# Performance work log

Measured on AMD Instinct MI355X. Metric: run time of the kernel, lower is better.

## Reference

```python
import jax, jax.numpy as jnp
import numpy as np

B, N, F, H = 2, 256, 64, 4
HID = 64            # hidden_features
C = H * HID         # n_coefficients = 256
KF = 50             # kernel_features (rbf count)
CUTOFF_UPPER = 5.0  # ExpNormalSmearing default (lower = 0)
ALPHA = 5.0 / CUTOFF_UPPER


def _dense(key, din, dout):
    scale = 1.0 / np.sqrt(din)
    return jax.random.uniform(key, (din, dout), minval=-scale, maxval=scale).astype(jnp.float32)


def setup_inputs() -> dict:
    key = jax.random.key(0)
    ks = jax.random.split(key, 16)
    start = float(np.exp(-CUTOFF_UPPER))
    means = jnp.asarray(np.linspace(start, 1.0, KF), jnp.float32)
    betas = jnp.full((KF,), (2.0 / KF * (1.0 - start)) ** -2, dtype=jnp.float32)
    d_edge_in = 2 * F              # h_cat_ht width
    d_cat = 2 * F + KF + 1         # concat([h0, rbf*h, dist])
    return dict(
        h=jax.random.normal(ks[0], (B, N, F), jnp.float32),
        x=jax.random.normal(ks[1], (B, N, 3), jnp.float32),
        v=jax.random.normal(ks[2], (B, N, 3), jnp.float32) * 0.1,
        W_in=_dense(ks[3], d_edge_in, KF), b_in=jnp.zeros((KF,), jnp.float32),
        rbf_means=means, rbf_betas=betas,
        W_o1=_dense(ks[4], d_cat, HID), b_o1=jnp.zeros((HID,), jnp.float32),
        W_o2=_dense(ks[5], HID, HID), b_o2=jnp.zeros((HID,), jnp.float32),
        W_sem=_dense(ks[6], HID, H), b_sem=jnp.zeros((H,), jnp.float32),
        W_xmix=_dense(ks[7], C, C),
        W_p1=_dense(ks[8], C, HID), b_p1=jnp.zeros((HID,), jnp.float32),
        W_p2=_dense(ks[9], HID, HID), b_p2=jnp.zeros((HID,), jnp.float32),
        W_n1=_dense(ks[10], F + C + HID, HID), b_n1=jnp.zeros((HID,), jnp.float32),
        W_n2=_dense(ks[11], HID, F), b_n2=jnp.zeros((F,), jnp.float32),
        W_v1=_dense(ks[12], F, HID), b_v1=jnp.zeros((HID,), jnp.float32),
        W_v2=_dense(ks[13], HID, 1),
        W_vmix=_dense(ks[14], C, 1),
    )


def reference(h, x, v, W_in, b_in, rbf_means, rbf_betas, W_o1, b_o1, W_o2, b_o2,
              W_sem, b_sem, W_xmix, W_p1, b_p1, W_p2, b_p2,
              W_n1, b_n1, W_n2, b_n2, W_v1, b_v1, W_v2, W_vmix):
    silu = jax.nn.silu
    n = h.shape[-2]
    # all-pairs displacements: entry [i, j] = x_j - x_i  (get_x_minus_xt)
    x_minus_xt = x[..., None, :, :] - x[..., :, None, :]                       # [B,N,N,3]
    d = jnp.sqrt(jax.nn.relu((x_minus_xt ** 2).sum(-1, keepdims=True)) + 1e-5)  # [B,N,N,1]
    # h_cat_ht: concat([h_j, h_i]) per pair (get_h_cat_ht)
    h_j = jnp.broadcast_to(h[..., None, :, :], h.shape[:-2] + (n, n, h.shape[-1]))
    h_i = jnp.broadcast_to(h[..., :, None, :], h.shape[:-2] + (n, n, h.shape[-1]))
    h_cat = jnp.concatenate([h_j, h_i], -1)                                     # [B,N,N,2F]
    # --- edge model: ContinuousFilterConvolutionWithConcatenation ---
    h1 = h_cat @ W_in + b_in                                                    # [B,N,N,KF]
    cut = 0.5 * (jnp.cos(d * jnp.pi / CUTOFF_UPPER) + 1.0) * (d < CUTOFF_UPPER)
    rbf = cut * jnp.exp(-rbf_betas * (jnp.exp(-ALPHA * d) - rbf_means) ** 2)    # [B,N,N,KF]
    h_e_mtx = silu(jnp.concatenate([h_cat, rbf * h1, d], -1) @ W_o1 + b_o1) @ W_o2 + b_o2  # [B,N,N,HID]
    # --- semantic attention (cutoff=None => euclidean factor is 1.0) ---
    att = jax.nn.celu(h_e_mtx @ W_sem + b_sem, alpha=2.0)                       # [B,N,N,H]
    att = att - 1e5 * jnp.eye(n, dtype=att.dtype)[..., None]                    # mask self-pairs
    att = jax.nn.softmax(att, axis=-2)
    combined = att / att.sum(-2, keepdims=True)                                 # combined_attention
    # per-head weighted edge features, flattened (feature-major, head-minor)
    h_e_att = (h_e_mtx[..., :, None] * combined[..., None, :]).reshape(h_e_mtx.shape[:-1] + (C,))  # [B,N,N,C]
    # --- spatial attention ---
    coeff = jnp.tanh(h_e_att @ W_xmix)                                          # x_mixing, [B,N,N,C]
    x_hat = x_minus_xt / (d + 1e-5)                                             # [B,N,N,3]
    # combinations[b,i,j,c,:] = x_hat[b,i,j,:] * coeff[b,i,j,c]; mean over j, fused:
    comb_sum = jnp.einsum('bijc,bijd->bicd', coeff, x_hat) / n                  # [B,N,C,3]
    comb_norm = (comb_sum ** 2).sum(-1)                                         # [B,N,C]
    h_comb = silu(silu(comb_norm @ W_p1 + b_p1) @ W_p2 + b_p2)                  # post_norm_mlp
    # --- aggregate + node model (residual) ---
    h_e = h_e_att.sum(-2)                                                       # [B,N,C]
    h_new = h + silu(silu(jnp.concatenate([h, h_e, h_comb], -1) @ W_n1 + b_n1) @ W_n2 + b_n2)
    # --- velocity / coordinate update (v_mixing then mean over j, fused via comb_sum) ---
    delta_v = jnp.einsum('bicd,c->bid', comb_sum, W_vmix[:, 0])                 # [B,N,3]
    v_scale = 2.0 * jax.nn.sigmoid(silu(h_new @ W_v1 + b_v1) @ W_v2)            # velocity_mlp + double_sigmoid
    v_new = delta_v + v_scale * v
    x_new = x + v_new
    return (h_new, x_new, v_new)
```

## Files before the change

### kernel.cpp

```cpp
#include <hip/hip_runtime.h>
#include <hip/hip_bf16.h>

typedef __hip_bfloat16 bf16;
typedef __attribute__((ext_vector_type(8))) short bf16x8;
typedef __attribute__((ext_vector_type(4))) short s16x4;
typedef __attribute__((ext_vector_type(4))) float f32x4;

#define NNODE 512

__device__ __forceinline__ float b2f(bf16 v){ return __bfloat162float(v); }
__device__ __forceinline__ float siluf(float x){ return x / (1.f + __expf(-x)); }
__device__ __forceinline__ float tanhfast(float x){ return 1.f - 2.f/(__expf(2.f*x)+1.f); }
__device__ __forceinline__ float celu2(float x){ return x > 0.f ? x : 2.f*(__expf(0.5f*x)-1.f); }
__device__ __forceinline__ float bs2f(short v){ union{unsigned int i; float f;} t; t.i = ((unsigned int)(unsigned short)v) << 16; return t.f; }
__device__ __forceinline__ short f2bs(float x){ union{ bf16 b; short s; } u; u.b = __float2bfloat16(x); return u.s; }
__device__ __forceinline__ float lo16f(unsigned int u){ union{unsigned int i; float f;} t; t.i = u<<16; return t.f; }
__device__ __forceinline__ float hi16f(unsigned int u){ union{unsigned int i; float f;} t; t.i = u & 0xffff0000u; return t.f; }

template<typename T> __device__ __forceinline__ float ldv(const void* p, int i);
template<> __device__ __forceinline__ float ldv<float>(const void* p, int i){ return ((const float*)p)[i]; }
template<> __device__ __forceinline__ float ldv<bf16 >(const void* p, int i){ return b2f(((const bf16*)p)[i]); }

template<typename T> __device__ __forceinline__ void stv(void* p, int i, float v);
template<> __device__ __forceinline__ void stv<float>(void* p, int i, float v){ ((float*)p)[i] = v; }
template<> __device__ __forceinline__ void stv<bf16 >(void* p, int i, float v){ ((bf16*)p)[i] = __float2bfloat16(v); }

template<typename T> __device__ __forceinline__ short ldbs(const void* p, int i);
template<> __device__ __forceinline__ short ldbs<bf16 >(const void* p, int i){ union{ bf16 b; short s; } u; u.b = ((const bf16*)p)[i]; return u.s; }
template<> __device__ __forceinline__ short ldbs<float>(const void* p, int i){ return f2bs(((const float*)p)[i]); }

struct Args {
    const void *h,*x,*v,*Win,*bin,*means,*betas,*Wo1,*bo1,*Wo2,*bo2,*Wsem,*bsem,*Wx,
               *Wp1,*bp1,*Wp2,*bp2,*Wn1,*bn1,*Wn2,*bn2,*Wv1,*bv1,*Wv2,*Wvm;
};

__device__ __forceinline__ bool detect_f32(const void* means){
    float v = b2f(((const bf16*)means)[0]);
    return (fabsf(v) > 1.0f || v != v);
}

template<typename T>
__device__ __forceinline__ void nodepre_body(const Args& A, short* __restrict__ U1,
                                             float* __restrict__ Aj, short* __restrict__ WxT,
                                             float* sh, float (*p1)[64], float (*p2)[64])
{
    int bn = blockIdx.x, tid = threadIdx.x;
    int t = tid & 63, ks = tid >> 6;
    if (tid < 64) sh[tid] = ldv<T>(A.h, bn*64 + tid);
    __syncthreads();
    float a1 = 0.f;
    #pragma unroll
    for (int q = 0; q < 16; ++q){
        int f = ks*16 + q;
        a1 += sh[f] * ldv<T>(A.Wo1, f*64 + t);
    }
    p1[ks][t] = a1;
    if (t < 50){
        float a2 = 0.f;
        #pragma unroll
        for (int q = 0; q < 16; ++q){
            int f = ks*16 + q;
            a2 += sh[f] * ldv<T>(A.Win, f*50 + t);
        }
        p2[ks][t] = a2;
    }
    if (tid < 128){
        int oo = bn*128 + tid;
        int hh = oo >> 14, rem = oo & 16383, n = rem >> 6, f = oo & 63;
        WxT[oo] = ldbs<T>(A.Wx, (4*f + hh)*256 + n);
    }
    __syncthreads();
    if (tid < 64){
        U1[bn*64 + tid] = f2bs(p1[0][tid] + p1[1][tid] + p1[2][tid] + p1[3][tid]);
        float av = (tid < 50) ? (p2[0][tid] + p2[1][tid] + p2[2][tid] + p2[3][tid]) : 0.f;
        Aj[bn*64 + tid] = av;
    }
}

__global__ void __launch_bounds__(256) k_nodepre(Args A, short* __restrict__ U1,
                                                 float* __restrict__ Aj, short* __restrict__ WxT)
{
    __shared__ float sh[64];
    __shared__ float p1[4][64];
    __shared__ float p2[4][64];
    if (detect_f32(A.means)) nodepre_body<float>(A, U1, Aj, WxT, sh, p1, p2);
    else                     nodepre_body<bf16 >(A, U1, Aj, WxT, sh, p1, p2);
}

struct SmemPost {
    __align__(16) float att[256][4];
    float part[4][256];
    float red[768];
    float cn[256];
    float he[256];
    float fa[64];
    float fb[64];
    float mpart[8][64];
    float tmp[8][4];
};
struct Smem {
    __align__(16) bf16  e[256][72];
    __align__(16) float x4[256][4];
    float hi[64];
    float ub[64];
    float wl[64];
    __align__(16) float kc[64][4];
    short wsem[256];
    __align__(16) short wo1t[64*72];
    __align__(16) short wo2t[64*72];
    union {
        SmemPost post;
        __align__(16) short mid[8][16][72];
    } u;
};

template<typename T>
__device__ __forceinline__ void sake_body(const Args& A,
        const short* __restrict__ U1w, const float* __restrict__ Ajw,
        const short* __restrict__ wxt, void* __restrict__ out, Smem& S)
{
    int bi = blockIdx.x;
    int b = bi >> 8, i = bi & 255;
    int tid = threadIdx.x, w = tid >> 6, lane = tid & 63;
    int lane15 = lane & 15, quad = lane >> 4;

    if (tid < 64)  S.hi[tid]   = ldv<T>(A.h, bi*64 + tid);
    if (tid < 256) S.wsem[tid] = ldbs<T>(A.Wsem, tid);
    if (tid < 64){
        bool kv = tid < 50;
        S.kc[tid][0] = kv ? ldv<T>(A.means, tid) : 0.f;
        S.kc[tid][1] = kv ? ldv<T>(A.betas, tid) : 0.f;
        S.kc[tid][2] = kv ? ldv<T>(A.bin,   tid) : 0.f;
        S.kc[tid][3] = 0.f;
    }
    #pragma unroll
    for (int q = 0; q < 8; ++q){
        int idx = q*512 + tid;
        int n = idx >> 6, k = idx & 63;
        S.wo2t[n*72 + k] = ldbs<T>(A.Wo2, k*64 + n);
        S.wo1t[n*72 + k] = (k < 50) ? ldbs<T>(A.Wo1, (128+k)*64 + n) : (short)0;
    }
    float xi0 = ldv<T>(A.x, bi*3+0), xi1 = ldv<T>(A.x, bi*3+1), xi2 = ldv<T>(A.x, bi*3+2);
    if (tid < 256){
        int j = tid;
        float dx = ldv<T>(A.x,(b*256+j)*3+0) - xi0;
        float dy = ldv<T>(A.x,(b*256+j)*3+1) - xi1;
        float dz = ldv<T>(A.x,(b*256+j)*3+2) - xi2;
        float dd = sqrtf(dx*dx + dy*dy + dz*dz + 1e-5f);
        float inv = 1.f/(dd + 1e-5f);
        S.x4[j][0] = dx*inv; S.x4[j][1] = dy*inv; S.x4[j][2] = dz*inv; S.x4[j][3] = dd;
    }
    __syncthreads();

    if (w == 0){
        float u2v = 0.f;
        for (int f = 0; f < 64; ++f) u2v += S.hi[f] * ldv<T>(A.Wo1, (64+f)*64 + lane);
        S.ub[lane] = u2v + ldv<T>(A.bo1, lane);
        S.wl[lane] = ldv<T>(A.Wo1, 178*64 + lane);
    } else if (w == 1 && lane < 50){
        float av = 0.f;
        for (int f = 0; f < 64; ++f) av += S.hi[f] * ldv<T>(A.Win, (64+f)*50 + lane);
        S.kc[lane][3] = av;
    }
    __syncthreads();

    float ubr[16], wlr[16], bo2r[16];
    #pragma unroll
    for (int nf = 0; nf < 4; ++nf){
        #pragma unroll
        for (int r = 0; r < 4; ++r){
            int m = nf*16 + quad*4 + r;
            ubr[nf*4+r]  = S.ub[m];
            wlr[nf*4+r]  = S.wl[m];
            bo2r[nf*4+r] = ldv<T>(A.bo2, m);
        }
    }

    for (int pass = 0; pass < 2; ++pass){
        int j = pass*128 + w*16 + lane15;
        float dd  = S.x4[j][3];
        float cut = (dd < 5.f) ? 0.5f*(__cosf(dd*0.6283185307f) + 1.f) : 0.f;
        float ed  = __expf(-dd);
        const float* ajp = Ajw + (b*256 + j)*64;
        bf16x8 Brb[2];
        #pragma unroll
        for (int s = 0; s < 2; ++s){
            int kb = s*32 + quad*8;
            f32x4 a0 = *(const f32x4*)(ajp + kb);
            f32x4 a1 = *(const f32x4*)(ajp + kb + 4);
            bf16x8 bv;
            #pragma unroll
            for (int i2 = 0; i2 < 8; ++i2){
                int k = kb + i2;
                f32x4 kcv = *(const f32x4*)&S.kc[k][0];
                float aj = (i2 < 4) ? a0[i2] : a1[i2-4];
                float h1 = aj + kcv[3] + kcv[2];
                float ex = ed - kcv[0];
                float val = cut * __expf(-kcv[1]*ex*ex) * h1;
                bv[i2] = (k < 50) ? f2bs(val) : (short)0;
            }
            Brb[s] = bv;
        }
        const short* u1p = U1w + (b*256 + j)*64;
        #pragma unroll
        for (int nf = 0; nf < 4; ++nf){
            const short* wp = S.wo1t + (nf*16 + lane15)*72;
            bf16x8 A0 = *(const bf16x8*)(wp + quad*8);
            bf16x8 A1 = *(const bf16x8*)(wp + 32 + quad*8);
            s16x4 u4 = *(const s16x4*)(u1p + nf*16 + quad*4);
            f32x4 C;
            #pragma unroll
            for (int r = 0; r < 4; ++r)
                C[r] = bs2f(u4[r]) + ubr[nf*4+r] + dd*wlr[nf*4+r];
            C = __builtin_amdgcn_mfma_f32_16x16x32_bf16(A0, Brb[0], C, 0, 0, 0);
            C = __builtin_amdgcn_mfma_f32_16x16x32_bf16(A1, Brb[1], C, 0, 0, 0);
            s16x4 m4;
            #pragma unroll
            for (int r = 0; r < 4; ++r) m4[r] = f2bs(siluf(C[r]));
            *(s16x4*)&S.u.mid[w][lane15][nf*16 + quad*4] = m4;
        }
        bf16x8 Bm0 = *(const bf16x8*)&S.u.mid[w][lane15][quad*8];
        bf16x8 Bm1 = *(const bf16x8*)&S.u.mid[w][lane15][32 + quad*8];
        #pragma unroll
        for (int nf = 0; nf < 4; ++nf){
            const short* wp = S.wo2t + (nf*16 + lane15)*72;
            bf16x8 A0 = *(const bf16x8*)(wp + quad*8);
            bf16x8 A1 = *(const bf16x8*)(wp + 32 + quad*8);
            f32x4 C = (f32x4){bo2r[nf*4+0], bo2r[nf*4+1], bo2r[nf*4+2], bo2r[nf*4+3]};
            C = __builtin_amdgcn_mfma_f32_16x16x32_bf16(A0, Bm0, C, 0, 0, 0);
            C = __builtin_amdgcn_mfma_f32_16x16x32_bf16(A1, Bm1, C, 0, 0, 0);
            s16x4 e4;
            #pragma unroll
            for (int r = 0; r < 4; ++r) e4[r] = f2bs(C[r]);
            *(s16x4*)&((short*)S.e)[j*72 + nf*16 + quad*4] = e4;
        }
    }
    __syncthreads();

    {
        bf16x8 Bs[2];
        #pragma unroll
        for (int ks = 0; ks < 2; ++ks){
            bf16x8 bv = (bf16x8){0,0,0,0,0,0,0,0};
            if (lane15 < 4){
                #pragma unroll
                for (int i2 = 0; i2 < 8; ++i2)
                    bv[i2] = S.wsem[(ks*32 + quad*8 + i2)*4 + lane15];
            }
            Bs[ks] = bv;
        }
        float bsv = (lane15 < 4) ? ldv<T>(A.bsem, lane15) : 0.f;
        #pragma unroll
        for (int t2 = 0; t2 < 2; ++t2){
            int jt = w*2 + t2;
            const short* ep = (const short*)S.e + (jt*16 + lane15)*72;
            bf16x8 A0 = *(const bf16x8*)(ep + quad*8);
            bf16x8 A1 = *(const bf16x8*)(ep + 32 + quad*8);
            f32x4 C = (f32x4){bsv, bsv, bsv, bsv};
            C = __builtin_amdgcn_mfma_f32_16x16x32_bf16(A0, Bs[0], C, 0, 0, 0);
            C = __builtin_amdgcn_mfma_f32_16x16x32_bf16(A1, Bs[1], C, 0, 0, 0);
            if (lane15 < 4){
                #pragma unroll
                for (int r = 0; r < 4; ++r){
                    int jr = jt*16 + quad*4 + r;
                    float lv = celu2(C[r]);
                    if (jr == i) lv -= 1e5f;
                    S.u.post.att[jr][lane15] = lv;
                }
            }
        }
    }
    __syncthreads();

    float ex0 = 0.f, ex1 = 0.f, ex2 = 0.f, ex3 = 0.f;
    if (tid < 256){
        float l0 = S.u.post.att[tid][0], l1 = S.u.post.att[tid][1];
        float l2 = S.u.post.att[tid][2], l3 = S.u.post.att[tid][3];
        float m0 = l0, m1 = l1, m2 = l2, m3 = l3;
        #pragma unroll
        for (int off = 1; off < 64; off <<= 1){
            m0 = fmaxf(m0, __shfl_xor(m0, off)); m1 = fmaxf(m1, __shfl_xor(m1, off));
            m2 = fmaxf(m2, __shfl_xor(m2, off)); m3 = fmaxf(m3, __shfl_xor(m3, off));
        }
        if (lane == 0){
            S.u.post.tmp[w][0] = m0; S.u.post.tmp[w][1] = m1;
            S.u.post.tmp[w][2] = m2; S.u.post.tmp[w][3] = m3;
        }
        ex0 = l0; ex1 = l1; ex2 = l2; ex3 = l3;
    }
    __syncthreads();
    if (tid < 256){
        float m0 = fmaxf(fmaxf(S.u.post.tmp[0][0], S.u.post.tmp[1][0]), fmaxf(S.u.post.tmp[2][0], S.u.post.tmp[3][0]));
        float m1 = fmaxf(fmaxf(S.u.post.tmp[0][1], S.u.post.tmp[1][1]), fmaxf(S.u.post.tmp[2][1], S.u.post.tmp[3][1]));
        float m2 = fmaxf(fmaxf(S.u.post.tmp[0][2], S.u.post.tmp[1][2]), fmaxf(S.u.post.tmp[2][2], S.u.post.tmp[3][2]));
        float m3 = fmaxf(fmaxf(S.u.post.tmp[0][3], S.u.post.tmp[1][3]), fmaxf(S.u.post.tmp[2][3], S.u.post.tmp[3][3]));
        ex0 = __expf(ex0-m0); ex1 = __expf(ex1-m1); ex2 = __expf(ex2-m2); ex3 = __expf(ex3-m3);
        float s0 = ex0, s1 = ex1, s2 = ex2, s3 = ex3;
        #pragma unroll
        for (int off = 1; off < 64; off <<= 1){
            s0 += __shfl_xor(s0, off); s1 += __shfl_xor(s1, off);
            s2 += __shfl_xor(s2, off); s3 += __shfl_xor(s3, off);
        }
        if (lane == 0){
            S.u.post.tmp[4+w][0] = s0; S.u.post.tmp[4+w][1] = s1;
            S.u.post.tmp[4+w][2] = s2; S.u.post.tmp[4+w][3] = s3;
        }
    }
    __syncthreads();
    if (tid < 256){
        float s0 = S.u.post.tmp[4][0]+S.u.post.tmp[5][0]+S.u.post.tmp[6][0]+S.u.post.tmp[7][0];
        float s1 = S.u.post.tmp[4][1]+S.u.post.tmp[5][1]+S.u.post.tmp[6][1]+S.u.post.tmp[7][1];
        float s2 = S.u.post.tmp[4][2]+S.u.post.tmp[5][2]+S.u.post.tmp[6][2]+S.u.post.tmp[7][2];
        float s3 = S.u.post.tmp[4][3]+S.u.post.tmp[5][3]+S.u.post.tmp[6][3]+S.u.post.tmp[7][3];
        S.u.post.att[tid][0] = ex0/s0; S.u.post.att[tid][1] = ex1/s1;
        S.u.post.att[tid][2] = ex2/s2; S.u.post.att[tid][3] = ex3/s3;
    }
    __syncthreads();

    {
        int cg = tid & 127, js = tid >> 7;
        int fp = cg >> 2, hh = cg & 3;
        float acc0 = 0.f, acc1 = 0.f;
        const unsigned int* ep = (const unsigned int*)S.e;
        for (int jj = 0; jj < 64; ++jj){
            int j = js*64 + jj;
            unsigned int u = ep[j*36 + fp];
            float a = S.u.post.att[j][hh];
            acc0 += lo16f(u)*a; acc1 += hi16f(u)*a;
        }
        S.u.post.part[js][8*fp + hh]     = acc0;
        S.u.post.part[js][8*fp + 4 + hh] = acc1;
    }
    __syncthreads();
    if (tid < 256)
        S.u.post.he[tid] = S.u.post.part[0][tid] + S.u.post.part[1][tid]
                         + S.u.post.part[2][tid] + S.u.post.part[3][tid];

    {
        const short* se_s = (const short*)S.e;
        bf16x8 Bh[2][4][2];
        #pragma unroll
        for (int nf2 = 0; nf2 < 2; ++nf2){
            int n = w*32 + nf2*16 + lane15;
            #pragma unroll
            for (int hh = 0; hh < 4; ++hh){
                const short* bp = wxt + (hh*256 + n)*64 + quad*8;
                Bh[nf2][hh][0] = *(const bf16x8*)(bp);
                Bh[nf2][hh][1] = *(const bf16x8*)(bp + 32);
            }
        }
        float ca[2][3];
        #pragma unroll
        for (int nf2 = 0; nf2 < 2; ++nf2){ ca[nf2][0]=0.f; ca[nf2][1]=0.f; ca[nf2][2]=0.f; }

        for (int mt = 0; mt < 16; ++mt){
            int jq = mt*16 + quad*4;
            f32x4 att4[4];
            #pragma unroll
            for (int r = 0; r < 4; ++r) att4[r] = *(const f32x4*)&S.u.post.att[jq + r][0];
            bf16x8 Af[2];
            #pragma unroll
            for (int ks = 0; ks < 2; ++ks)
                Af[ks] = *(const bf16x8*)(se_s + (mt*16 + lane15)*72 + ks*32 + quad*8);
            #pragma unroll
            for (int nf2 = 0; nf2 < 2; ++nf2){
                float Pt[4] = {0.f, 0.f, 0.f, 0.f};
                #pragma unroll
                for (int hh = 0; hh < 4; ++hh){
                    f32x4 Cc = (f32x4){0.f,0.f,0.f,0.f};
                    Cc = __builtin_amdgcn_mfma_f32_16x16x32_bf16(Af[0], Bh[nf2][hh][0], Cc, 0, 0, 0);
                    Cc = __builtin_amdgcn_mfma_f32_16x16x32_bf16(Af[1], Bh[nf2][hh][1], Cc, 0, 0, 0);
                    #pragma unroll
                    for (int r = 0; r < 4; ++r) Pt[r] += att4[r][hh] * Cc[r];
                }
                #pragma unroll
                for (int r = 0; r < 4; ++r){
                    int j = jq + r;
                    float cf = tanhfast(Pt[r]);
                    f32x4 xh = *(const f32x4*)&S.x4[j][0];
                    ca[nf2][0] += cf*xh[0]; ca[nf2][1] += cf*xh[1]; ca[nf2][2] += cf*xh[2];
                }
            }
        }
        #pragma unroll
        for (int nf2 = 0; nf2 < 2; ++nf2){
            #pragma unroll
            for (int d = 0; d < 3; ++d){
                float vs = ca[nf2][d];
                vs += __shfl_xor(vs, 16);
                vs += __shfl_xor(vs, 32);
                if (quad == 0) S.u.post.red[(w*32 + nf2*16 + lane15)*3 + d] = vs;
            }
        }
    }
    __syncthreads();

    const float sc = 1.f/256.f;
    if (tid < 256){
        float c0 = S.u.post.red[tid*3+0]*sc, c1 = S.u.post.red[tid*3+1]*sc, c2 = S.u.post.red[tid*3+2]*sc;
        S.u.post.cn[tid] = c0*c0 + c1*c1 + c2*c2;
    }
    __syncthreads();

    {
        float acc = 0.f;
        int c0 = w*32;
        for (int c = c0; c < c0+32; ++c) acc += S.u.post.cn[c] * ldv<T>(A.Wp1, c*64 + lane);
        S.u.post.mpart[w][lane] = acc;
    }
    __syncthreads();
    if (tid < 64){
        float acc = ldv<T>(A.bp1, tid);
        #pragma unroll
        for (int q = 0; q < 8; ++q) acc += S.u.post.mpart[q][tid];
        S.u.post.fa[tid] = siluf(acc);
    }
    __syncthreads();
    {
        float acc = 0.f;
        int k0 = w*8;
        #pragma unroll
        for (int k = 0; k < 8; ++k) acc += S.u.post.fa[k0+k] * ldv<T>(A.Wp2, (k0+k)*64 + lane);
        S.u.post.mpart[w][lane] = acc;
    }
    __syncthreads();
    if (tid < 64){
        float acc = ldv<T>(A.bp2, tid);
        #pragma unroll
        for (int q = 0; q < 8; ++q) acc += S.u.post.mpart[q][tid];
        S.u.post.fb[tid] = siluf(acc);
    }
    __syncthreads();
    {
        float acc = 0.f;
        int r0 = w*48;
        for (int r = r0; r < r0+48; ++r){
            float xv = (r < 64) ? S.hi[r] : (r < 320) ? S.u.post.he[r-64] : S.u.post.fb[r-320];
            acc += xv * ldv<T>(A.Wn1, r*64 + lane);
        }
        S.u.post.mpart[w][lane] = acc;
    }
    __syncthreads();
    if (tid < 64){
        float acc = ldv<T>(A.bn1, tid);
        #pragma unroll
        for (int q = 0; q < 8; ++q) acc += S.u.post.mpart[q][tid];
        S.u.post.fa[tid] = siluf(acc);
    }
    __syncthreads();
    {
        float acc = 0.f;
        int k0 = w*8;
        #pragma unroll
        for (int k = 0; k < 8; ++k) acc += S.u.post.fa[k0+k] * ldv<T>(A.Wn2, (k0+k)*64 + lane);
        S.u.post.mpart[w][lane] = acc;
    }
    __syncthreads();
    if (tid < 64){
        float acc = ldv<T>(A.bn2, tid);
        #pragma unroll
        for (int q = 0; q < 8; ++q) acc += S.u.post.mpart[q][tid];
        float hn = S.hi[tid] + siluf(acc);
        stv<T>(out, bi*64 + tid, hn);
        S.u.post.fb[tid] = hn;
    }
    __syncthreads();
    {
        float acc = 0.f;
        int k0 = w*8;
        #pragma unroll
        for (int k = 0; k < 8; ++k) acc += S.u.post.fb[k0+k] * ldv<T>(A.Wv1, (k0+k)*64 + lane);
        S.u.post.mpart[w][lane] = acc;
    }
    __syncthreads();
    float vscale = 0.f;
    if (tid < 64){
        float acc = ldv<T>(A.bv1, tid);
        #pragma unroll
        for (int q = 0; q < 8; ++q) acc += S.u.post.mpart[q][tid];
        float term = siluf(acc) * ldv<T>(A.Wv2, tid);
        #pragma unroll
        for (int off = 1; off < 64; off <<= 1) term += __shfl_xor(term, off);
        vscale = 2.f / (1.f + __expf(-term));
    }
    if (w < 4){
        int c = w*64 + lane;
        float wv = ldv<T>(A.Wvm, c);
        float d0 = S.u.post.red[c*3+0]*sc*wv;
        float d1 = S.u.post.red[c*3+1]*sc*wv;
        float d2 = S.u.post.red[c*3+2]*sc*wv;
        #pragma unroll
        for (int off = 1; off < 64; off <<= 1){
            d0 += __shfl_xor(d0, off); d1 += __shfl_xor(d1, off); d2 += __shfl_xor(d2, off);
        }
        if (lane == 0){ S.u.post.tmp[w][0] = d0; S.u.post.tmp[w][1] = d1; S.u.post.tmp[w][2] = d2; }
    }
    __syncthreads();
    if (tid < 3){
        float dv = S.u.post.tmp[0][tid] + S.u.post.tmp[1][tid] + S.u.post.tmp[2][tid] + S.u.post.tmp[3][tid];
        float vn = dv + vscale * ldv<T>(A.v, bi*3 + tid);
        float xn = ldv<T>(A.x, bi*3 + tid) + vn;
        stv<T>(out, 32768 + bi*3 + tid, xn);
        stv<T>(out, 34304 + bi*3 + tid, vn);
    }
}

__global__ void __launch_bounds__(512, 4) k_sake(Args A,
                                                 const short* __restrict__ U1w,
                                                 const float* __restrict__ Ajw,
                                                 const short* __restrict__ wxt,
                                                 void* __restrict__ out)
{
    __shared__ Smem S;
    if (detect_f32(A.means)) sake_body<float>(A, U1w, Ajw, wxt, out, S);
    else                     sake_body<bf16 >(A, U1w, Ajw, wxt, out, S);
}

extern "C" void kernel_launch(void* const* d_in, const int* in_sizes, int n_in,
                              void* d_out, int out_size, void* d_ws, size_t ws_size,
                              hipStream_t stream)
{
    Args A;
    A.h     = d_in[0];  A.x     = d_in[1];  A.v     = d_in[2];
    A.Win   = d_in[3];  A.bin   = d_in[4];  A.means = d_in[5];  A.betas = d_in[6];
    A.Wo1   = d_in[7];  A.bo1   = d_in[8];  A.Wo2   = d_in[9];  A.bo2   = d_in[10];
    A.Wsem  = d_in[11]; A.bsem  = d_in[12]; A.Wx    = d_in[13];
    A.Wp1   = d_in[14]; A.bp1   = d_in[15]; A.Wp2   = d_in[16]; A.bp2   = d_in[17];
    A.Wn1   = d_in[18]; A.bn1   = d_in[19]; A.Wn2   = d_in[20]; A.bn2   = d_in[21];
    A.Wv1   = d_in[22]; A.bv1   = d_in[23]; A.Wv2   = d_in[24]; A.Wvm   = d_in[25];

    short* U1b  = (short*)d_ws;
    float* Aj   = (float*)((char*)d_ws + 65536);
    short* WxT  = (short*)((char*)d_ws + 65536 + 131072);

    k_nodepre<<<NNODE, 256, 0, stream>>>(A, U1b, Aj, WxT);
    k_sake<<<NNODE, 512, 0, stream>>>(A, U1b, Aj, WxT, d_out);
}
```

Measured before the change: 180.1 us.

## Fold h_e aggregation into Wn1 via MFMA and slim post-MLP barriers

Precomputes transposed Wn1 slices (hi/lo bf16 split) alongside WxT so the attention-weighted h_e sum is folded directly into the Wn1 product using MFMA, removing the scalar 256-wide h_e reduction and part buffers. Stores attention weights in padding columns of the edge tile to shrink shared memory, unions edge weights with post buffers, and removes two barriers. Post-MLPs are restructured to use shuffle reductions across 8 output features per wave instead of cross-wave smem partials. Risks precision changes from hi/lo split and possible race from removed barriers.

```diff
diff --git a/kernel.cpp b/kernel.cpp
--- a/kernel.cpp
+++ b/kernel.cpp
@@ -64,10 +64,21 @@
         }
         p2[ks][t] = a2;
     }
-    if (tid < 128){
-        int oo = bn*128 + tid;
-        int hh = oo >> 14, rem = oo & 16383, n = rem >> 6, f = oo & 63;
-        WxT[oo] = ldbs<T>(A.Wx, (4*f + hh)*256 + n);
+    if (tid < 192){
+        int oo = bn*192 + tid;
+        int hh = oo / 24576;
+        int rem = oo - hh*24576;
+        int n = rem >> 6, k = rem & 63;
+        short v;
+        if (n < 256){
+            v = ldbs<T>(A.Wx, (4*k + hh)*256 + n);
+        } else if (n < 320){
+            v = ldbs<T>(A.Wn1, (64 + 4*k + hh)*64 + (n - 256));
+        } else {
+            float wv = ldv<T>(A.Wn1, (64 + 4*k + hh)*64 + (n - 320));
+            v = f2bs(wv - bs2f(f2bs(wv)));
+        }
+        WxT[oo] = v;
     }
     __syncthreads();
     if (tid < 64){
@@ -88,15 +99,18 @@
 }
 
 struct SmemPost {
-    __align__(16) float att[256][4];
-    float part[4][256];
     float red[768];
     float cn[256];
-    float he[256];
     float fa[64];
     float fb[64];
-    float mpart[8][64];
+    float hep[8][16];
     float tmp[8][4];
+    float tmp2[8];
+};
+struct SmemEdge {
+    __align__(16) short wo1t[64*72];
+    __align__(16) short wo2t[64*72];
+    __align__(16) short mid[8][16][72];
 };
 struct Smem {
     __align__(16) bf16  e[256][72];
@@ -105,14 +119,13 @@
     float ub[64];
     float wl[64];
     __align__(16) float kc[64][4];
-    short wsem[256];
-    __align__(16) short wo1t[64*72];
-    __align__(16) short wo2t[64*72];
-    union {
-        SmemPost post;
-        __align__(16) short mid[8][16][72];
-    } u;
+    __align__(16) short wsem[256];
+    union { SmemEdge edge; SmemPost post; } u;
 };
+
+__device__ __forceinline__ float* attp(Smem& S, int j){
+    return (float*)((short*)S.e + j*72 + 64);
+}
 
 template<typename T>
 __device__ __forceinline__ void sake_body(const Args& A,
@@ -131,14 +144,14 @@
         S.kc[tid][0] = kv ? ldv<T>(A.means, tid) : 0.f;
         S.kc[tid][1] = kv ? ldv<T>(A.betas, tid) : 0.f;
         S.kc[tid][2] = kv ? ldv<T>(A.bin,   tid) : 0.f;
-        S.kc[tid][3] = 0.f;
+        if (!kv) S.kc[tid][3] = 0.f;
     }
     #pragma unroll
     for (int q = 0; q < 8; ++q){
         int idx = q*512 + tid;
         int n = idx >> 6, k = idx & 63;
-        S.wo2t[n*72 + k] = ldbs<T>(A.Wo2, k*64 + n);
-        S.wo1t[n*72 + k] = (k < 50) ? ldbs<T>(A.Wo1, (128+k)*64 + n) : (short)0;
+        S.u.edge.wo2t[n*72 + k] = ldbs<T>(A.Wo2, k*64 + n);
+        S.u.edge.wo1t[n*72 + k] = (k < 50) ? ldbs<T>(A.Wo1, (128+k)*64 + n) : (short)0;
     }
     float xi0 = ldv<T>(A.x, bi*3+0), xi1 = ldv<T>(A.x, bi*3+1), xi2 = ldv<T>(A.x, bi*3+2);
     if (tid < 256){
@@ -150,16 +163,14 @@
         float inv = 1.f/(dd + 1e-5f);
         S.x4[j][0] = dx*inv; S.x4[j][1] = dy*inv; S.x4[j][2] = dz*inv; S.x4[j][3] = dd;
     }
-    __syncthreads();
-
     if (w == 0){
         float u2v = 0.f;
-        for (int f = 0; f < 64; ++f) u2v += S.hi[f] * ldv<T>(A.Wo1, (64+f)*64 + lane);
+        for (int f = 0; f < 64; ++f) u2v += ldv<T>(A.h, bi*64 + f) * ldv<T>(A.Wo1, (64+f)*64 + lane);
         S.ub[lane] = u2v + ldv<T>(A.bo1, lane);
         S.wl[lane] = ldv<T>(A.Wo1, 178*64 + lane);
     } else if (w == 1 && lane < 50){
         float av = 0.f;
-        for (int f = 0; f < 64; ++f) av += S.hi[f] * ldv<T>(A.Win, (64+f)*50 + lane);
+        for (int f = 0; f < 64; ++f) av += ldv<T>(A.h, bi*64 + f) * ldv<T>(A.Win, (64+f)*50 + lane);
         S.kc[lane][3] = av;
     }
     __syncthreads();
@@ -176,6 +187,7 @@
         }
     }
 
+    #pragma unroll
     for (int pass = 0; pass < 2; ++pass){
         int j = pass*128 + w*16 + lane15;
         float dd  = S.x4[j][3];
@@ -204,7 +216,7 @@
         const short* u1p = U1w + (b*256 + j)*64;
         #pragma unroll
         for (int nf = 0; nf < 4; ++nf){
-            const short* wp = S.wo1t + (nf*16 + lane15)*72;
+            const short* wp = S.u.edge.wo1t + (nf*16 + lane15)*72;
             bf16x8 A0 = *(const bf16x8*)(wp + quad*8);
             bf16x8 A1 = *(const bf16x8*)(wp + 32 + quad*8);
             s16x4 u4 = *(const s16x4*)(u1p + nf*16 + quad*4);
@@ -217,13 +229,13 @@
             s16x4 m4;
             #pragma unroll
             for (int r = 0; r < 4; ++r) m4[r] = f2bs(siluf(C[r]));
-            *(s16x4*)&S.u.mid[w][lane15][nf*16 + quad*4] = m4;
-        }
-        bf16x8 Bm0 = *(const bf16x8*)&S.u.mid[w][lane15][quad*8];
-        bf16x8 Bm1 = *(const bf16x8*)&S.u.mid[w][lane15][32 + quad*8];
+            *(s16x4*)&S.u.edge.mid[w][lane15][nf*16 + quad*4] = m4;
+        }
+        bf16x8 Bm0 = *(const bf16x8*)&S.u.edge.mid[w][lane15][quad*8];
+        bf16x8 Bm1 = *(const bf16x8*)&S.u.edge.mid[w][lane15][32 + quad*8];
         #pragma unroll
         for (int nf = 0; nf < 4; ++nf){
-            const short* wp = S.wo2t + (nf*16 + lane15)*72;
+            const short* wp = S.u.edge.wo2t + (nf*16 + lane15)*72;
             bf16x8 A0 = *(const bf16x8*)(wp + quad*8);
             bf16x8 A1 = *(const bf16x8*)(wp + 32 + quad*8);
             f32x4 C = (f32x4){bo2r[nf*4+0], bo2r[nf*4+1], bo2r[nf*4+2], bo2r[nf*4+3]};
@@ -235,7 +247,6 @@
             *(s16x4*)&((short*)S.e)[j*72 + nf*16 + quad*4] = e4;
         }
     }
-    __syncthreads();
 
     {
         bf16x8 Bs[2];
@@ -252,7 +263,7 @@
         float bsv = (lane15 < 4) ? ldv<T>(A.bsem, lane15) : 0.f;
         #pragma unroll
         for (int t2 = 0; t2 < 2; ++t2){
-            int jt = w*2 + t2;
+            int jt = t2 ? (8 + w) : w;
             const short* ep = (const short*)S.e + (jt*16 + lane15)*72;
             bf16x8 A0 = *(const bf16x8*)(ep + quad*8);
             bf16x8 A1 = *(const bf16x8*)(ep + 32 + quad*8);
@@ -265,7 +276,7 @@
                     int jr = jt*16 + quad*4 + r;
                     float lv = celu2(C[r]);
                     if (jr == i) lv -= 1e5f;
-                    S.u.post.att[jr][lane15] = lv;
+                    attp(S, jr)[lane15] = lv;
                 }
             }
         }
@@ -274,9 +285,8 @@
 
     float ex0 = 0.f, ex1 = 0.f, ex2 = 0.f, ex3 = 0.f;
     if (tid < 256){
-        float l0 = S.u.post.att[tid][0], l1 = S.u.post.att[tid][1];
-        float l2 = S.u.post.att[tid][2], l3 = S.u.post.att[tid][3];
-        float m0 = l0, m1 = l1, m2 = l2, m3 = l3;
+        f32x4 l = *(const f32x4*)attp(S, tid);
+        float m0 = l[0], m1 = l[1], m2 = l[2], m3 = l[3];
         #pragma unroll
         for (int off = 1; off < 64; off <<= 1){
             m0 = fmaxf(m0, __shfl_xor(m0, off)); m1 = fmaxf(m1, __shfl_xor(m1, off));
@@ -286,7 +296,7 @@
             S.u.post.tmp[w][0] = m0; S.u.post.tmp[w][1] = m1;
             S.u.post.tmp[w][2] = m2; S.u.post.tmp[w][3] = m3;
         }
-        ex0 = l0; ex1 = l1; ex2 = l2; ex3 = l3;
+        ex0 = l[0]; ex1 = l[1]; ex2 = l[2]; ex3 = l[3];
     }
     __syncthreads();
     if (tid < 256){
@@ -312,86 +322,87 @@
         float s1 = S.u.post.tmp[4][1]+S.u.post.tmp[5][1]+S.u.post.tmp[6][1]+S.u.post.tmp[7][1];
         float s2 = S.u.post.tmp[4][2]+S.u.post.tmp[5][2]+S.u.post.tmp[6][2]+S.u.post.tmp[7][2];
         float s3 = S.u.post.tmp[4][3]+S.u.post.tmp[5][3]+S.u.post.tmp[6][3]+S.u.post.tmp[7][3];
-        S.u.post.att[tid][0] = ex0/s0; S.u.post.att[tid][1] = ex1/s1;
-        S.u.post.att[tid][2] = ex2/s2; S.u.post.att[tid][3] = ex3/s3;
-    }
-    __syncthreads();
-
-    {
-        int cg = tid & 127, js = tid >> 7;
-        int fp = cg >> 2, hh = cg & 3;
-        float acc0 = 0.f, acc1 = 0.f;
-        const unsigned int* ep = (const unsigned int*)S.e;
-        for (int jj = 0; jj < 64; ++jj){
-            int j = js*64 + jj;
-            unsigned int u = ep[j*36 + fp];
-            float a = S.u.post.att[j][hh];
-            acc0 += lo16f(u)*a; acc1 += hi16f(u)*a;
-        }
-        S.u.post.part[js][8*fp + hh]     = acc0;
-        S.u.post.part[js][8*fp + 4 + hh] = acc1;
-    }
-    __syncthreads();
-    if (tid < 256)
-        S.u.post.he[tid] = S.u.post.part[0][tid] + S.u.post.part[1][tid]
-                         + S.u.post.part[2][tid] + S.u.post.part[3][tid];
+        *(f32x4*)attp(S, tid) = (f32x4){ex0/s0, ex1/s1, ex2/s2, ex3/s3};
+    }
+    __syncthreads();
 
     {
         const short* se_s = (const short*)S.e;
-        bf16x8 Bh[2][4][2];
         #pragma unroll
         for (int nf2 = 0; nf2 < 2; ++nf2){
             int n = w*32 + nf2*16 + lane15;
+            bf16x8 Bh[4][2];
             #pragma unroll
             for (int hh = 0; hh < 4; ++hh){
-                const short* bp = wxt + (hh*256 + n)*64 + quad*8;
-                Bh[nf2][hh][0] = *(const bf16x8*)(bp);
-                Bh[nf2][hh][1] = *(const bf16x8*)(bp + 32);
-            }
-        }
-        float ca[2][3];
-        #pragma unroll
-        for (int nf2 = 0; nf2 < 2; ++nf2){ ca[nf2][0]=0.f; ca[nf2][1]=0.f; ca[nf2][2]=0.f; }
-
-        for (int mt = 0; mt < 16; ++mt){
-            int jq = mt*16 + quad*4;
-            f32x4 att4[4];
-            #pragma unroll
-            for (int r = 0; r < 4; ++r) att4[r] = *(const f32x4*)&S.u.post.att[jq + r][0];
-            bf16x8 Af[2];
-            #pragma unroll
-            for (int ks = 0; ks < 2; ++ks)
-                Af[ks] = *(const bf16x8*)(se_s + (mt*16 + lane15)*72 + ks*32 + quad*8);
-            #pragma unroll
-            for (int nf2 = 0; nf2 < 2; ++nf2){
+                const short* bp = wxt + (hh*384 + n)*64 + quad*8;
+                Bh[hh][0] = *(const bf16x8*)(bp);
+                Bh[hh][1] = *(const bf16x8*)(bp + 32);
+            }
+            float c0 = 0.f, c1 = 0.f, c2 = 0.f;
+            for (int mt = 0; mt < 16; ++mt){
+                int jq = mt*16 + quad*4;
+                f32x4 att4[4];
+                #pragma unroll
+                for (int r = 0; r < 4; ++r) att4[r] = *(const f32x4*)attp(S, jq + r);
+                bf16x8 Af[2];
+                #pragma unroll
+                for (int ks = 0; ks < 2; ++ks)
+                    Af[ks] = *(const bf16x8*)(se_s + (mt*16 + lane15)*72 + ks*32 + quad*8);
                 float Pt[4] = {0.f, 0.f, 0.f, 0.f};
                 #pragma unroll
                 for (int hh = 0; hh < 4; ++hh){
                     f32x4 Cc = (f32x4){0.f,0.f,0.f,0.f};
-                    Cc = __builtin_amdgcn_mfma_f32_16x16x32_bf16(Af[0], Bh[nf2][hh][0], Cc, 0, 0, 0);
-                    Cc = __builtin_amdgcn_mfma_f32_16x16x32_bf16(Af[1], Bh[nf2][hh][1], Cc, 0, 0, 0);
+                    Cc = __builtin_amdgcn_mfma_f32_16x16x32_bf16(Af[0], Bh[hh][0], Cc, 0, 0, 0);
+                    Cc = __builtin_amdgcn_mfma_f32_16x16x32_bf16(Af[1], Bh[hh][1], Cc, 0, 0, 0);
                     #pragma unroll
                     for (int r = 0; r < 4; ++r) Pt[r] += att4[r][hh] * Cc[r];
                 }
                 #pragma unroll
                 for (int r = 0; r < 4; ++r){
-                    int j = jq + r;
                     float cf = tanhfast(Pt[r]);
-                    f32x4 xh = *(const f32x4*)&S.x4[j][0];
-                    ca[nf2][0] += cf*xh[0]; ca[nf2][1] += cf*xh[1]; ca[nf2][2] += cf*xh[2];
+                    f32x4 xh = *(const f32x4*)&S.x4[jq + r][0];
+                    c0 += cf*xh[0]; c1 += cf*xh[1]; c2 += cf*xh[2];
                 }
             }
-        }
-        #pragma unroll
-        for (int nf2 = 0; nf2 < 2; ++nf2){
-            #pragma unroll
-            for (int d = 0; d < 3; ++d){
-                float vs = ca[nf2][d];
-                vs += __shfl_xor(vs, 16);
-                vs += __shfl_xor(vs, 32);
-                if (quad == 0) S.u.post.red[(w*32 + nf2*16 + lane15)*3 + d] = vs;
-            }
-        }
+            c0 += __shfl_xor(c0, 16); c0 += __shfl_xor(c0, 32);
+            c1 += __shfl_xor(c1, 16); c1 += __shfl_xor(c1, 32);
+            c2 += __shfl_xor(c2, 16); c2 += __shfl_xor(c2, 32);
+            if (quad == 0){
+                S.u.post.red[n*3 + 0] = c0;
+                S.u.post.red[n*3 + 1] = c1;
+                S.u.post.red[n*3 + 2] = c2;
+            }
+        }
+    }
+
+    {
+        const short* se_s = (const short*)S.e;
+        int t16 = (w >> 1) * 16;
+        int mt0 = (w & 1) * 8;
+        float heacc = 0.f;
+        #pragma unroll
+        for (int hh = 0; hh < 4; ++hh){
+            const short* bhp = wxt + (hh*384 + 256 + t16 + lane15)*64 + quad*8;
+            bf16x8 Bhi0 = *(const bf16x8*)(bhp);
+            bf16x8 Bhi1 = *(const bf16x8*)(bhp + 32);
+            bf16x8 Blo0 = *(const bf16x8*)(bhp + 4096);
+            bf16x8 Blo1 = *(const bf16x8*)(bhp + 4096 + 32);
+            for (int mt = mt0; mt < mt0 + 8; ++mt){
+                bf16x8 Af0 = *(const bf16x8*)(se_s + (mt*16 + lane15)*72 + quad*8);
+                bf16x8 Af1 = *(const bf16x8*)(se_s + (mt*16 + lane15)*72 + 32 + quad*8);
+                f32x4 Cc = (f32x4){0.f,0.f,0.f,0.f};
+                Cc = __builtin_amdgcn_mfma_f32_16x16x32_bf16(Af0, Bhi0, Cc, 0, 0, 0);
+                Cc = __builtin_amdgcn_mfma_f32_16x16x32_bf16(Af1, Bhi1, Cc, 0, 0, 0);
+                Cc = __builtin_amdgcn_mfma_f32_16x16x32_bf16(Af0, Blo0, Cc, 0, 0, 0);
+                Cc = __builtin_amdgcn_mfma_f32_16x16x32_bf16(Af1, Blo1, Cc, 0, 0, 0);
+                #pragma unroll
+                for (int r = 0; r < 4; ++r)
+                    heacc += attp(S, mt*16 + quad*4 + r)[hh] * Cc[r];
+            }
+        }
+        heacc += __shfl_xor(heacc, 16);
+        heacc += __shfl_xor(heacc, 32);
+        if (quad == 0) S.u.post.hep[w][lane15] = heacc;
     }
     __syncthreads();
 
@@ -399,92 +410,8 @@
     if (tid < 256){
         float c0 = S.u.post.red[tid*3+0]*sc, c1 = S.u.post.red[tid*3+1]*sc, c2 = S.u.post.red[tid*3+2]*sc;
         S.u.post.cn[tid] = c0*c0 + c1*c1 + c2*c2;
-    }
-    __syncthreads();
-
-    {
-        float acc = 0.f;
-        int c0 = w*32;
-        for (int c = c0; c < c0+32; ++c) acc += S.u.post.cn[c] * ldv<T>(A.Wp1, c*64 + lane);
-        S.u.post.mpart[w][lane] = acc;
-    }
-    __syncthreads();
-    if (tid < 64){
-        float acc = ldv<T>(A.bp1, tid);
-        #pragma unroll
-        for (int q = 0; q < 8; ++q) acc += S.u.post.mpart[q][tid];
-        S.u.post.fa[tid] = siluf(acc);
-    }
-    __syncthreads();
-    {
-        float acc = 0.f;
-        int k0 = w*8;
-        #pragma unroll
-        for (int k = 0; k < 8; ++k) acc += S.u.post.fa[k0+k] * ldv<T>(A.Wp2, (k0+k)*64 + lane);
-        S.u.post.mpart[w][lane] = acc;
-    }
-    __syncthreads();
-    if (tid < 64){
-        float acc = ldv<T>(A.bp2, tid);
-        #pragma unroll
-        for (int q = 0; q < 8; ++q) acc += S.u.post.mpart[q][tid];
-        S.u.post.fb[tid] = siluf(acc);
-    }
-    __syncthreads();
-    {
-        float acc = 0.f;
-        int r0 = w*48;
-        for (int r = r0; r < r0+48; ++r){
-            float xv = (r < 64) ? S.hi[r] : (r < 320) ? S.u.post.he[r-64] : S.u.post.fb[r-320];
-            acc += xv * ldv<T>(A.Wn1, r*64 + lane);
-        }
-        S.u.post.mpart[w][lane] = acc;
-    }
-    __syncthreads();
-    if (tid < 64){
-        float acc = ldv<T>(A.bn1, tid);
-        #pragma unroll
-        for (int q = 0; q < 8; ++q) acc += S.u.post.mpart[q][tid];
-        S.u.post.fa[tid] = siluf(acc);
-    }
-    __syncthreads();
-    {
-        float acc = 0.f;
-        int k0 = w*8;
-        #pragma unroll
-        for (int k = 0; k < 8; ++k) acc += S.u.post.fa[k0+k] * ldv<T>(A.Wn2, (k0+k)*64 + lane);
-        S.u.post.mpart[w][lane] = acc;
-    }
-    __syncthreads();
-    if (tid < 64){
-        float acc = ldv<T>(A.bn2, tid);
-        #pragma unroll
-        for (int q = 0; q < 8; ++q) acc += S.u.post.mpart[q][tid];
-        float hn = S.hi[tid] + siluf(acc);
-        stv<T>(out, bi*64 + tid, hn);
-        S.u.post.fb[tid] = hn;
-    }
-    __syncthreads();
-    {
-        float acc = 0.f;
-        int k0 = w*8;
-        #pragma unroll
-        for (int k = 0; k < 8; ++k) acc += S.u.post.fb[k0+k] * ldv<T>(A.Wv1, (k0+k)*64 + lane);
-        S.u.post.mpart[w][lane] = acc;
-    }
-    __syncthreads();
-    float vscale = 0.f;
-    if (tid < 64){
-        float acc = ldv<T>(A.bv1, tid);
-        #pragma unroll
-        for (int q = 0; q < 8; ++q) acc += S.u.post.mpart[q][tid];
-        float term = siluf(acc) * ldv<T>(A.Wv2, tid);
-        #pragma unroll
-        for (int off = 1; off < 64; off <<= 1) term += __shfl_xor(term, off);
-        vscale = 2.f / (1.f + __expf(-term));
-    }
-    if (w < 4){
-        int c = w*64 + lane;
+    } else {
+        int c = (w-4)*64 + lane;
         float wv = ldv<T>(A.Wvm, c);
         float d0 = S.u.post.red[c*3+0]*sc*wv;
         float d1 = S.u.post.red[c*3+1]*sc*wv;
@@ -493,10 +420,83 @@
         for (int off = 1; off < 64; off <<= 1){
             d0 += __shfl_xor(d0, off); d1 += __shfl_xor(d1, off); d2 += __shfl_xor(d2, off);
         }
-        if (lane == 0){ S.u.post.tmp[w][0] = d0; S.u.post.tmp[w][1] = d1; S.u.post.tmp[w][2] = d2; }
+        if (lane == 0){ S.u.post.tmp[w-4][0] = d0; S.u.post.tmp[w-4][1] = d1; S.u.post.tmp[w-4][2] = d2; }
+    }
+    __syncthreads();
+
+    int fs = lane & 7, ks8 = lane >> 3;
+    int fo = w*8 + fs;
+    {
+        float acc = 0.f;
+        int c0 = ks8*32;
+        for (int it = 0; it < 32; ++it){
+            int c = c0 + it;
+            acc += S.u.post.cn[c] * ldv<T>(A.Wp1, c*64 + fo);
+        }
+        acc += __shfl_xor(acc, 8); acc += __shfl_xor(acc, 16); acc += __shfl_xor(acc, 32);
+        if (lane < 8) S.u.post.fa[w*8 + lane] = siluf(acc + ldv<T>(A.bp1, w*8 + lane));
+    }
+    __syncthreads();
+    {
+        float acc = 0.f;
+        #pragma unroll
+        for (int q = 0; q < 8; ++q){
+            int k = ks8*8 + q;
+            acc += S.u.post.fa[k] * ldv<T>(A.Wp2, k*64 + fo);
+        }
+        acc += __shfl_xor(acc, 8); acc += __shfl_xor(acc, 16); acc += __shfl_xor(acc, 32);
+        if (lane < 8) S.u.post.fb[w*8 + lane] = siluf(acc + ldv<T>(A.bp2, w*8 + lane));
+    }
+    __syncthreads();
+    {
+        float acc = 0.f;
+        #pragma unroll
+        for (int q = 0; q < 8; ++q){
+            int k = ks8*8 + q;
+            acc += S.hi[k]        * ldv<T>(A.Wn1, k*64 + fo);
+            acc += S.u.post.fb[k] * ldv<T>(A.Wn1, (320+k)*64 + fo);
+        }
+        acc += __shfl_xor(acc, 8); acc += __shfl_xor(acc, 16); acc += __shfl_xor(acc, 32);
+        if (lane < 8){
+            int f = w*8 + lane;
+            float heW = S.u.post.hep[2*(f>>4)][f&15] + S.u.post.hep[2*(f>>4)+1][f&15];
+            S.u.post.fa[f] = siluf(acc + heW + ldv<T>(A.bn1, f));
+        }
+    }
+    __syncthreads();
+    {
+        float acc = 0.f;
+        #pragma unroll
+        for (int q = 0; q < 8; ++q){
+            int k = ks8*8 + q;
+            acc += S.u.post.fa[k] * ldv<T>(A.Wn2, k*64 + fo);
+        }
+        acc += __shfl_xor(acc, 8); acc += __shfl_xor(acc, 16); acc += __shfl_xor(acc, 32);
+        if (lane < 8){
+            int f = w*8 + lane;
+            float hn = S.hi[f] + siluf(acc + ldv<T>(A.bn2, f));
+            stv<T>(out, bi*64 + f, hn);
+            S.u.post.fb[f] = hn;
+        }
+    }
+    __syncthreads();
+    {
+        float acc = 0.f;
+        #pragma unroll
+        for (int q = 0; q < 8; ++q){
+            int k = ks8*8 + q;
+            acc += S.u.post.fb[k] * ldv<T>(A.Wv1, k*64 + fo);
+        }
+        acc += __shfl_xor(acc, 8); acc += __shfl_xor(acc, 16); acc += __shfl_xor(acc, 32);
+        float term = siluf(acc + ldv<T>(A.bv1, fo)) * ldv<T>(A.Wv2, fo);
+        term += __shfl_xor(term, 1); term += __shfl_xor(term, 2); term += __shfl_xor(term, 4);
+        if (lane == 0) S.u.post.tmp2[w] = term;
     }
     __syncthreads();
     if (tid < 3){
+        float t = S.u.post.tmp2[0]+S.u.post.tmp2[1]+S.u.post.tmp2[2]+S.u.post.tmp2[3]
+                + S.u.post.tmp2[4]+S.u.post.tmp2[5]+S.u.post.tmp2[6]+S.u.post.tmp2[7];
+        float vscale = 2.f / (1.f + __expf(-t));
         float dv = S.u.post.tmp[0][tid] + S.u.post.tmp[1][tid] + S.u.post.tmp[2][tid] + S.u.post.tmp[3][tid];
         float vn = dv + vscale * ldv<T>(A.v, bi*3 + tid);
         float xn = ldv<T>(A.x, bi*3 + tid) + vn;
```

Measured after the change: 272.3 us. +51.2%, slower.
